# Optimization experiments

Hardware: AMD Instinct MI355X
Metric: run time of the kernel (lower is better)

The kernel has to match this reference:

```python
import jax, jax.numpy as jnp
import numpy as np

FILTERS = 64
HIDDEN = 128
T_PRED = 24
DILATIONS = (1, 2, 4, 8, 16, 32)
N_DIL = len(DILATIONS)
FEAT = 15
B = 1024
L_ENC = 168


def setup_inputs() -> dict:
    key = jax.random.key(0)
    ks = jax.random.split(key, 16)
    s = 0.05
    d_in = 1 + FEAT  # prev_output (1) concat current feature
    inp = {
        "decoder_features": jax.random.normal(ks[0], (B, T_PRED, FEAT), jnp.float32),
        "decoder_init_input": jax.random.normal(ks[1], (B, 1), jnp.float32),
        "encoder_states": jax.random.normal(ks[2], (N_DIL, B, L_ENC, FILTERS), jnp.float32),
        # dense_1: d_in -> filters (tanh)
        "W1": jax.random.normal(ks[3], (d_in, FILTERS), jnp.float32) * s,
        "b1": jnp.zeros((FILTERS,), jnp.float32),
        # dense_2: filters -> 2*filters (bias)
        "W2": jax.random.normal(ks[4], (FILTERS, 2 * FILTERS), jnp.float32) * s,
        "b2": jnp.zeros((2 * FILTERS,), jnp.float32),
        # dense_3: filters -> 2*filters (no bias)
        "W3": jax.random.normal(ks[5], (FILTERS, 2 * FILTERS), jnp.float32) * s,
        # dense_4: filters -> 2*filters (bias)
        "W4": jax.random.normal(ks[6], (FILTERS, 2 * FILTERS), jnp.float32) * s,
        "b4": jnp.zeros((2 * FILTERS,), jnp.float32),
        # dense_5: n_dil*filters -> hidden (relu)
        "W5": jax.random.normal(ks[7], (N_DIL * FILTERS, HIDDEN), jnp.float32) * s,
        "b5": jnp.zeros((HIDDEN,), jnp.float32),
        # dense_6: hidden -> 1
        "W6": jax.random.normal(ks[8], (HIDDEN, 1), jnp.float32) * s,
        "b6": jnp.zeros((1,), jnp.float32),
    }
    return inp


def _decode(decoder_features, decoder_init_input, encoder_states,
            W1, b1, W2, b2, W3, W4, b4, W5, b5, W6, b6):
    L = encoder_states.shape[2]
    # 'appended' holds the inputs written back into each dilation's state
    # (the growing-concat part of encoder_states in the original loop).
    appended0 = jnp.zeros((N_DIL, decoder_features.shape[0], T_PRED, FILTERS),
                          dtype=decoder_features.dtype)

    def step(carry, t):
        prev, appended = carry
        cur = jnp.concatenate([prev, decoder_features[:, t, :]], axis=1)  # [B, 1+FEAT]
        inputs = jnp.tanh(cur @ W1 + b1)  # [B, F]
        skips_list = []
        for i, d in enumerate(DILATIONS):
            # grown-state read index is (L + t) - d; if t >= d it lands in the
            # appended region (step t-d), otherwise in the original encoder state.
            idx_app = jnp.clip(t - d, 0, T_PRED - 1)
            idx_orig = jnp.clip(L + t - d, 0, L - 1)
            st_app = jax.lax.dynamic_index_in_dim(appended[i], idx_app, axis=1, keepdims=False)
            st_orig = jax.lax.dynamic_index_in_dim(encoder_states[i], idx_orig, axis=1, keepdims=False)
            state = jnp.where(t >= d, st_app, st_orig)  # [B, F]
            dilated = state @ W2 + b2 + inputs @ W3  # [B, 2F]
            conv_filter, conv_gate = dilated[:, :FILTERS], dilated[:, FILTERS:]
            gated = jnp.tanh(conv_filter) * jax.nn.sigmoid(conv_gate)
            out = gated @ W4 + b4  # [B, 2F]
            skips, residuals = out[:, :FILTERS], out[:, FILTERS:]
            inputs = inputs + residuals
            appended = appended.at[i, :, t, :].set(inputs)
            skips_list.append(skips)
        skip = jax.nn.relu(jnp.concatenate(skips_list, axis=1))  # [B, N_DIL*F]
        h = jax.nn.relu(skip @ W5 + b5)
        y = h @ W6 + b6  # [B, 1]
        return (y, appended), y

    (_, _), ys = jax.lax.scan(step, (decoder_init_input, appended0),
                              jnp.arange(T_PRED))
    return jnp.transpose(ys, (1, 0, 2))  # [B, T, 1]


def reference(decoder_features, decoder_init_input, encoder_states,
              W1, b1, W2, b2, W3, W4, b4, W5, b5, W6, b6):
    return _decode(decoder_features, decoder_init_input, encoder_states,
                   W1, b1, W2, b2, W3, W4, b4, W5, b5, W6, b6)
```

## Files before the change

### kernel.cpp

```cpp
#include <hip/hip_runtime.h>

typedef _Float16 h16;
typedef _Float16 half8 __attribute__((ext_vector_type(8)));
typedef float floatx4 __attribute__((ext_vector_type(4)));

#define B_TOT 1024
#define T_STEPS 24
#define F 64
#define C2 128
#define FEAT 15
#define L_ENC 168
#define HID 128
#define R 16
#define BLK 256
#define FP 72

__device__ __forceinline__ floatx4 mfma16(half8 a, half8 b, floatx4 c) {
  return __builtin_amdgcn_mfma_f32_16x16x32_f16(a, b, c, 0, 0, 0);
}

#define BAR() asm volatile("s_waitcnt lgkmcnt(0)\n\ts_barrier" ::: "memory")

__device__ __forceinline__ float tanh_fast(float x) {
  float cx = fminf(fmaxf(x, -15.f), 15.f);
  float e  = __builtin_amdgcn_exp2f(-2.885390081777927f * cx);
  return (1.f - e) * __builtin_amdgcn_rcpf(1.f + e);
}
__device__ __forceinline__ float gate_fast(float f, float g) {
  float cf = fminf(fmaxf(f, -15.f), 15.f);
  float cg = fminf(fmaxf(g, -30.f), 30.f);
  float ef = __builtin_amdgcn_exp2f(-2.885390081777927f * cf);
  float eg = __builtin_amdgcn_exp2f(-1.4426950408889634f * cg);
  return (1.f - ef) * __builtin_amdgcn_rcpf((1.f + ef) * (1.f + eg));
}

__global__ void prep_w5(const float* __restrict__ gW5, h16* __restrict__ wsW5) {
  int t = blockIdx.x * 256 + threadIdx.x;
  if (t >= 12 * 8 * 64) return;
  int lane = t & 63, nt = (t >> 6) & 7, ktg = t >> 9;
  int n  = nt * 16 + (lane & 15);
  int kb = ktg * 32 + (lane >> 4) * 8;
  half8 v;
  #pragma unroll
  for (int j = 0; j < 8; ++j) v[j] = (h16)gW5[(size_t)(kb + j) * C2 + n];
  *(half8*)&wsW5[(size_t)t * 8] = v;
}

__global__ __launch_bounds__(BLK, 1) void decoder_v7(
    const float* __restrict__ dec_feat,
    const float* __restrict__ dec_init,
    const float* __restrict__ enc,
    const float* __restrict__ gW1, const float* __restrict__ gb1,
    const float* __restrict__ gW2, const float* __restrict__ gb2,
    const float* __restrict__ gW3,
    const float* __restrict__ gW4, const float* __restrict__ gb4,
    const h16*  __restrict__ wsW5, const float* __restrict__ gb5,
    const float* __restrict__ gW6, const float* __restrict__ gb6,
    float* __restrict__ out)
{
  __shared__ alignas(16) h16 ringL[31][R][FP];
  __shared__ alignas(16) h16 xH[R][FP];
  __shared__ alignas(16) h16 gatedH[R][FP];
  __shared__ alignas(16) h16 skipH[R][FP];
  __shared__ alignas(16) h16 curH[R][40];
  __shared__ float ypart[4][R];

  const int tid  = threadIdx.x;
  const int w    = tid >> 6;
  const int lane = tid & 63;
  const int m16  = lane & 15;
  const int q    = lane >> 4;
  const int q8   = q * 8;
  const int b0   = blockIdx.x * R;
  const int col  = w * 16 + m16;
  const int mm0  = tid / FEAT;
  const int f0   = tid - mm0 * FEAT;
  const bool featT = (tid < R * FEAT);

  half8 rW1;
  #pragma unroll
  for (int j = 0; j < 8; ++j) {
    int k = q8 + j;
    rW1[j] = (k < 16) ? (h16)gW1[k * F + col] : (h16)0.0f;
  }
  half8 rW2[2][2], rW3[2][2], rW4[2][2];
  #pragma unroll
  for (int h = 0; h < 2; ++h) {
    int n = (w + 4 * h) * 16 + m16;
    #pragma unroll
    for (int kt = 0; kt < 2; ++kt) {
      half8 v2, v3, v4;
      #pragma unroll
      for (int j = 0; j < 8; ++j) {
        int k = kt * 32 + q8 + j;
        v2[j] = (h16)gW2[k * C2 + n];
        v3[j] = (h16)gW3[k * C2 + n];
        v4[j] = (h16)gW4[k * C2 + n];
      }
      rW2[h][kt] = v2; rW3[h][kt] = v3; rW4[h][kt] = v4;
    }
  }
  half8 w5r[6][4];
  #pragma unroll
  for (int i = 0; i < 6; ++i)
    #pragma unroll
    for (int kt = 0; kt < 2; ++kt)
      #pragma unroll
      for (int nn = 0; nn < 2; ++nn)
        w5r[i][kt * 2 + nn] =
            *(const half8*)&wsW5[(size_t)((((2 * i + kt) * 8) + (w + 4 * nn)) * 64 + lane) * 8];

  const float rb1  = gb1[col];
  const float rb2f = gb2[col], rb2g = gb2[64 + col];
  const float rb4s = gb4[col], rb4r = gb4[64 + col];
  const float rb5a = gb5[col], rb5b = gb5[64 + col];
  const float rw6a = gW6[col], rw6b = gW6[64 + col];
  const float rb6  = gb6[0];

  { int mm = tid >> 4, kk = 16 + (tid & 15); curH[mm][kk] = (h16)0.0f; }
  if (featT) curH[mm0][1 + f0] = (h16)dec_feat[(b0 + mm0) * (T_STEPS * FEAT) + f0];
  if (tid < R) curH[tid][0] = (h16)dec_init[b0 + tid];
  __syncthreads();

  const int rbase[6] = {0, 1, 3, 7, 15, 0};

  auto loadStat = [&](half8* dst, int i, int d, int base, int t) {
    if (t >= d) {
      const h16* p = &ringL[base + (t & (d - 1))][m16][0];
      dst[0] = *(const half8*)(p + q8);
      dst[1] = *(const half8*)(p + 32 + q8);
    } else {
      const float* ep = enc + (((size_t)i * B_TOT + b0 + m16) * L_ENC + (L_ENC + t - d)) * F;
      #pragma unroll
      for (int kt = 0; kt < 2; ++kt) {
        float4 e0 = *(const float4*)(ep + kt * 32 + q8);
        float4 e1 = *(const float4*)(ep + kt * 32 + q8 + 4);
        half8 hv;
        hv[0] = (h16)e0.x; hv[1] = (h16)e0.y; hv[2] = (h16)e0.z; hv[3] = (h16)e0.w;
        hv[4] = (h16)e1.x; hv[5] = (h16)e1.y; hv[6] = (h16)e1.z; hv[7] = (h16)e1.w;
        dst[kt] = hv;
      }
    }
  };

  float xr[4];

  for (int t = 0; t < T_STEPS; ++t) {
    float nf = 0.f;
    const bool doFeat = featT && (t + 1 < T_STEPS);
    if (doFeat) nf = dec_feat[(b0 + mm0) * (T_STEPS * FEAT) + (t + 1) * FEAT + f0];

    half8 aCur = *(const half8*)&curH[m16][q8];
    floatx4 accX = {0.f, 0.f, 0.f, 0.f};
    accX = mfma16(aCur, rW1, accX);
    half8 stat[2];
    loadStat(stat, 0, 1, 0, t);
    #pragma unroll
    for (int j = 0; j < 4; ++j) {
      float v = tanh_fast(accX[j] + rb1);
      xr[j] = v;
      xH[q * 4 + j][col] = (h16)v;
    }
    BAR();

    floatx4 hAccA = {0.f, 0.f, 0.f, 0.f};
    floatx4 hAccB = {0.f, 0.f, 0.f, 0.f};

    #pragma unroll
    for (int i = 0; i < 6; ++i) {
      const int d = 1 << i;
      half8 xA0 = *(const half8*)&xH[m16][q8];
      half8 xA1 = *(const half8*)&xH[m16][32 + q8];
      half8 stN[2];
      if (i < 5) loadStat(stN, i + 1, d << 1, rbase[i + 1], t);

      floatx4 aF = {0.f, 0.f, 0.f, 0.f}, aG = {0.f, 0.f, 0.f, 0.f};
      aF = mfma16(stat[0], rW2[0][0], aF);
      aF = mfma16(stat[1], rW2[0][1], aF);
      aF = mfma16(xA0,     rW3[0][0], aF);
      aF = mfma16(xA1,     rW3[0][1], aF);
      aG = mfma16(stat[0], rW2[1][0], aG);
      aG = mfma16(stat[1], rW2[1][1], aG);
      aG = mfma16(xA0,     rW3[1][0], aG);
      aG = mfma16(xA1,     rW3[1][1], aG);
      #pragma unroll
      for (int j = 0; j < 4; ++j)
        gatedH[q * 4 + j][col] = (h16)gate_fast(aF[j] + rb2f, aG[j] + rb2g);
      BAR();

      half8 gA0 = *(const half8*)&gatedH[m16][q8];
      half8 gA1 = *(const half8*)&gatedH[m16][32 + q8];
      floatx4 oS = {0.f, 0.f, 0.f, 0.f}, oR = {0.f, 0.f, 0.f, 0.f};
      oS = mfma16(gA0, rW4[0][0], oS);
      oS = mfma16(gA1, rW4[0][1], oS);
      oR = mfma16(gA0, rW4[1][0], oR);
      oR = mfma16(gA1, rW4[1][1], oR);
      #pragma unroll
      for (int j = 0; j < 4; ++j) {
        int row = q * 4 + j;
        float s = oS[j] + rb4s;
        skipH[row][col] = (h16)fmaxf(s, 0.0f);
        float xn = xr[j] + oR[j] + rb4r;
        xr[j] = xn;
        h16 hx = (h16)xn;
        xH[row][col] = hx;
        if (i < 5) ringL[rbase[i] + (t & (d - 1))][row][col] = hx;
      }
      BAR();

      half8 sk0 = *(const half8*)&skipH[m16][q8];
      half8 sk1 = *(const half8*)&skipH[m16][32 + q8];
      hAccA = mfma16(sk0, w5r[i][0], hAccA);
      hAccA = mfma16(sk1, w5r[i][2], hAccA);
      hAccB = mfma16(sk0, w5r[i][1], hAccB);
      hAccB = mfma16(sk1, w5r[i][3], hAccB);

      if (i < 5) { stat[0] = stN[0]; stat[1] = stN[1]; }
    }

    {
      floatx4 vv;
      #pragma unroll
      for (int j = 0; j < 4; ++j) {
        float ha = fmaxf(hAccA[j] + rb5a, 0.0f);
        float hb = fmaxf(hAccB[j] + rb5b, 0.0f);
        vv[j] = ha * rw6a + hb * rw6b;
      }
      #pragma unroll
      for (int off = 1; off < 16; off <<= 1) {
        #pragma unroll
        for (int j = 0; j < 4; ++j) vv[j] += __shfl_xor(vv[j], off, 16);
      }
      if (m16 == 0) {
        #pragma unroll
        for (int j = 0; j < 4; ++j) ypart[w][q * 4 + j] = vv[j];
      }
    }
    if (doFeat) curH[mm0][1 + f0] = (h16)nf;
    BAR();
    if (tid < R) {
      float y = ypart[0][tid] + ypart[1][tid] + ypart[2][tid] + ypart[3][tid] + rb6;
      out[(b0 + tid) * T_STEPS + t] = y;
      curH[tid][0] = (h16)y;
    }
    BAR();
  }
}

extern "C" void kernel_launch(void* const* d_in, const int* in_sizes, int n_in,
                              void* d_out, int out_size, void* d_ws, size_t ws_size,
                              hipStream_t stream) {
  const float* dec_feat = (const float*)d_in[0];
  const float* dec_init = (const float*)d_in[1];
  const float* enc      = (const float*)d_in[2];
  const float* W1 = (const float*)d_in[3];
  const float* b1 = (const float*)d_in[4];
  const float* W2 = (const float*)d_in[5];
  const float* b2 = (const float*)d_in[6];
  const float* W3 = (const float*)d_in[7];
  const float* W4 = (const float*)d_in[8];
  const float* b4 = (const float*)d_in[9];
  const float* W5 = (const float*)d_in[10];
  const float* b5 = (const float*)d_in[11];
  const float* W6 = (const float*)d_in[12];
  const float* b6 = (const float*)d_in[13];
  float* out = (float*)d_out;
  h16* wsW5 = (h16*)d_ws;

  prep_w5<<<24, 256, 0, stream>>>(W5, wsW5);
  decoder_v7<<<dim3(B_TOT / R), dim3(BLK), 0, stream>>>(
      dec_feat, dec_init, enc, W1, b1, W2, b2, W3, W4, b4, wsW5, b5, W6, b6, out);
}
```

Baseline: 471.5 us.

## Preload encoder states and features into LDS, drop per-step barrier

All encoder states the decoder will read (the ring-buffer seeds for dilations 1-16 and all 24 steps of dilation 32) and all decoder features are prefetched into shared memory as fp16 before the time loop. Global loads inside the serial recurrence are removed. The y feedback is now recomputed by every lane from a transposed partial-sum buffer, which removes one barrier per step. Shared memory use grows noticeably, and the block is still limited to one per CU by the launch bounds.

```diff
diff --git a/kernel.cpp b/kernel.cpp
--- a/kernel.cpp
+++ b/kernel.cpp
@@ -1,6 +1,7 @@
 #include <hip/hip_runtime.h>
 
 typedef _Float16 h16;
+typedef _Float16 half4 __attribute__((ext_vector_type(4)));
 typedef _Float16 half8 __attribute__((ext_vector_type(8)));
 typedef float floatx4 __attribute__((ext_vector_type(4)));
 
@@ -46,7 +47,7 @@
   *(half8*)&wsW5[(size_t)t * 8] = v;
 }
 
-__global__ __launch_bounds__(BLK, 1) void decoder_v7(
+__global__ __launch_bounds__(BLK, 1) void decoder_v9(
     const float* __restrict__ dec_feat,
     const float* __restrict__ dec_init,
     const float* __restrict__ enc,
@@ -59,11 +60,12 @@
     float* __restrict__ out)
 {
   __shared__ alignas(16) h16 ringL[31][R][FP];
+  __shared__ alignas(16) h16 enc5L[T_STEPS][R][FP];
   __shared__ alignas(16) h16 xH[R][FP];
   __shared__ alignas(16) h16 gatedH[R][FP];
   __shared__ alignas(16) h16 skipH[R][FP];
-  __shared__ alignas(16) h16 curH[R][40];
-  __shared__ float ypart[4][R];
+  __shared__ alignas(16) h16 featH[T_STEPS][R][16];
+  __shared__ alignas(16) float ypartS[R][4];
 
   const int tid  = threadIdx.x;
   const int w    = tid >> 6;
@@ -73,9 +75,6 @@
   const int q8   = q * 8;
   const int b0   = blockIdx.x * R;
   const int col  = w * 16 + m16;
-  const int mm0  = tid / FEAT;
-  const int f0   = tid - mm0 * FEAT;
-  const bool featT = (tid < R * FEAT);
 
   half8 rW1;
   #pragma unroll
@@ -116,45 +115,74 @@
   const float rb5a = gb5[col], rb5b = gb5[64 + col];
   const float rw6a = gW6[col], rw6b = gW6[64 + col];
   const float rb6  = gb6[0];
-
-  { int mm = tid >> 4, kk = 16 + (tid & 15); curH[mm][kk] = (h16)0.0f; }
-  if (featT) curH[mm0][1 + f0] = (h16)dec_feat[(b0 + mm0) * (T_STEPS * FEAT) + f0];
-  if (tid < R) curH[tid][0] = (h16)dec_init[b0 + tid];
+  const float rInit = dec_init[b0 + m16];
+
+  {
+    int mm = tid >> 4, kk = (tid & 15) * 4;
+    #pragma unroll 1
+    for (int it = 0; it < 55; ++it) {
+      int i, s; h16* dst;
+      if (it < 31) {
+        i = (it >= 15) ? 4 : (it >= 7) ? 3 : (it >= 3) ? 2 : (it >= 1) ? 1 : 0;
+        s = it - ((1 << i) - 1);
+        dst = &ringL[it][mm][kk];
+      } else { i = 5; s = it - 31; dst = &enc5L[s][mm][kk]; }
+      int d = 1 << i;
+      const float* sp = enc + (((size_t)i * B_TOT + b0 + mm) * L_ENC + (L_ENC + s - d)) * F + kk;
+      float4 v = *(const float4*)sp;
+      half4 hv; hv[0] = (h16)v.x; hv[1] = (h16)v.y; hv[2] = (h16)v.z; hv[3] = (h16)v.w;
+      *(half4*)dst = hv;
+    }
+  }
+  for (int p = tid; p < T_STEPS * R; p += BLK) {
+    int tt = p >> 4, row = p & 15;
+    const float* sp = dec_feat + (size_t)(b0 + row) * (T_STEPS * FEAT) + tt * FEAT;
+    half8 v0, v1;
+    v0[0] = (h16)0.0f;
+    #pragma unroll
+    for (int j = 0; j < 7; ++j) v0[1 + j] = (h16)sp[j];
+    #pragma unroll
+    for (int j = 0; j < 8; ++j) v1[j] = (h16)sp[7 + j];
+    *(half8*)&featH[tt][row][0] = v0;
+    *(half8*)&featH[tt][row][8] = v1;
+  }
   __syncthreads();
 
-  const int rbase[6] = {0, 1, 3, 7, 15, 0};
-
-  auto loadStat = [&](half8* dst, int i, int d, int base, int t) {
-    if (t >= d) {
-      const h16* p = &ringL[base + (t & (d - 1))][m16][0];
-      dst[0] = *(const half8*)(p + q8);
-      dst[1] = *(const half8*)(p + 32 + q8);
+  auto loadStat = [&](half8* dst, int i, int t) {
+    const h16* p;
+    if (i == 5) p = &enc5L[t][m16][0];
+    else {
+      const int d = 1 << i;
+      p = &ringL[((1 << i) - 1) + (t & (d - 1))][m16][0];
+    }
+    dst[0] = *(const half8*)(p + q8);
+    dst[1] = *(const half8*)(p + 32 + q8);
+  };
+
+  float xr[4];
+
+  for (int t = 0; t < T_STEPS; ++t) {
+    float yv;
+    if (t == 0) yv = rInit;
+    else {
+      float4 yp = *(const float4*)&ypartS[m16][0];
+      yv = (yp.x + yp.y + yp.z + yp.w) + rb6;
+    }
+    if (t > 0 && w == 0 && q == 0)
+      out[(size_t)(b0 + m16) * T_STEPS + (t - 1)] = yv;
+
+    half8 aCur;
+    if (q < 2) {
+      aCur = *(const half8*)&featH[t][m16][q8];
     } else {
-      const float* ep = enc + (((size_t)i * B_TOT + b0 + m16) * L_ENC + (L_ENC + t - d)) * F;
-      #pragma unroll
-      for (int kt = 0; kt < 2; ++kt) {
-        float4 e0 = *(const float4*)(ep + kt * 32 + q8);
-        float4 e1 = *(const float4*)(ep + kt * 32 + q8 + 4);
-        half8 hv;
-        hv[0] = (h16)e0.x; hv[1] = (h16)e0.y; hv[2] = (h16)e0.z; hv[3] = (h16)e0.w;
-        hv[4] = (h16)e1.x; hv[5] = (h16)e1.y; hv[6] = (h16)e1.z; hv[7] = (h16)e1.w;
-        dst[kt] = hv;
-      }
-    }
-  };
-
-  float xr[4];
-
-  for (int t = 0; t < T_STEPS; ++t) {
-    float nf = 0.f;
-    const bool doFeat = featT && (t + 1 < T_STEPS);
-    if (doFeat) nf = dec_feat[(b0 + mm0) * (T_STEPS * FEAT) + (t + 1) * FEAT + f0];
-
-    half8 aCur = *(const half8*)&curH[m16][q8];
+      #pragma unroll
+      for (int j = 0; j < 8; ++j) aCur[j] = (h16)0.0f;
+    }
+    if (q == 0) aCur[0] = (h16)yv;
     floatx4 accX = {0.f, 0.f, 0.f, 0.f};
     accX = mfma16(aCur, rW1, accX);
     half8 stat[2];
-    loadStat(stat, 0, 1, 0, t);
+    loadStat(stat, 0, t);
     #pragma unroll
     for (int j = 0; j < 4; ++j) {
       float v = tanh_fast(accX[j] + rb1);
@@ -172,7 +200,7 @@
       half8 xA0 = *(const half8*)&xH[m16][q8];
       half8 xA1 = *(const half8*)&xH[m16][32 + q8];
       half8 stN[2];
-      if (i < 5) loadStat(stN, i + 1, d << 1, rbase[i + 1], t);
+      if (i < 5) loadStat(stN, i + 1, t);
 
       floatx4 aF = {0.f, 0.f, 0.f, 0.f}, aG = {0.f, 0.f, 0.f, 0.f};
       aF = mfma16(stat[0], rW2[0][0], aF);
@@ -204,7 +232,7 @@
         xr[j] = xn;
         h16 hx = (h16)xn;
         xH[row][col] = hx;
-        if (i < 5) ringL[rbase[i] + (t & (d - 1))][row][col] = hx;
+        if (i < 5) ringL[((1 << i) - 1) + (t & (d - 1))][row][col] = hx;
       }
       BAR();
 
@@ -233,17 +261,17 @@
       }
       if (m16 == 0) {
         #pragma unroll
-        for (int j = 0; j < 4; ++j) ypart[w][q * 4 + j] = vv[j];
-      }
-    }
-    if (doFeat) curH[mm0][1 + f0] = (h16)nf;
+        for (int j = 0; j < 4; ++j) ypartS[q * 4 + j][w] = vv[j];
+      }
+    }
     BAR();
-    if (tid < R) {
-      float y = ypart[0][tid] + ypart[1][tid] + ypart[2][tid] + ypart[3][tid] + rb6;
-      out[(b0 + tid) * T_STEPS + t] = y;
-      curH[tid][0] = (h16)y;
-    }
-    BAR();
+  }
+
+  {
+    float4 yp = *(const float4*)&ypartS[m16][0];
+    float yv = (yp.x + yp.y + yp.z + yp.w) + rb6;
+    if (w == 0 && q == 0)
+      out[(size_t)(b0 + m16) * T_STEPS + (T_STEPS - 1)] = yv;
   }
 }
 
@@ -268,6 +296,6 @@
   h16* wsW5 = (h16*)d_ws;
 
   prep_w5<<<24, 256, 0, stream>>>(W5, wsW5);
-  decoder_v7<<<dim3(B_TOT / R), dim3(BLK), 0, stream>>>(
+  decoder_v9<<<dim3(B_TOT / R), dim3(BLK), 0, stream>>>(
       dec_feat, dec_init, enc, W1, b1, W2, b2, W3, W4, b4, wsW5, b5, W6, b6, out);
 }
```

Result: faster. 447.2 us (-5.1%).
